# Performance work log

Hardware: AMD Instinct MI355X
Metric: run time of the kernel (lower is better)

## Reference

```python
import jax, jax.numpy as jnp
import numpy as np

D_MODEL = 1024
N_HEAD = 16
ATT_DIM = D_MODEL // N_HEAD  # 64
B, S = 8, 2048


def setup_inputs() -> dict:
    key = jax.random.key(0)
    kq, kk, kv, kwq, kwk, kwv = jax.random.split(key, 6)
    # xavier_uniform bound for Linear(hidden_dim -> att_dim)
    bound = float(np.sqrt(6.0 / (D_MODEL + ATT_DIM)))
    return {
        "q": jax.random.normal(kq, (B, S, D_MODEL), dtype=jnp.float32),
        "k": jax.random.normal(kk, (B, S, D_MODEL), dtype=jnp.float32),
        "v": jax.random.normal(kv, (B, S, D_MODEL), dtype=jnp.float32),
        "Wq": jax.random.uniform(kwq, (ATT_DIM, D_MODEL), jnp.float32, -bound, bound),
        "Wk": jax.random.uniform(kwk, (ATT_DIM, D_MODEL), jnp.float32, -bound, bound),
        "Wv": jax.random.uniform(kwv, (ATT_DIM, D_MODEL), jnp.float32, -bound, bound),
    }


def reference(q, k, v, Wq, Wk, Wv):
    # Linear projections (no bias): [B,S,d_model] @ [d_model,att_dim]
    qp = jnp.einsum('bsd,ed->bse', q, Wq)
    kp = jnp.einsum('bsd,ed->bse', k, Wk)
    vp = jnp.einsum('bsd,ed->bse', v, Wv)
    # Scores: note original divides by att_dim (not sqrt)
    scores = jnp.einsum('bqe,bke->bqk', qp, kp) / ATT_DIM
    probs = jax.nn.softmax(scores, axis=-1)  # [B,S,S]
    att = jnp.einsum('bqk,bke->bqe', probs, vp)  # [B,S,att_dim]
    # dropout is identity in eval mode
    return (att, probs)
```

## Files before the change

kernel.cpp:

```cpp
#include <hip/hip_runtime.h>
#include <hip/hip_bf16.h>

#define D_MODEL 1024
#define ATT_DIM 64
#define BATCH 8
#define SEQ 2048
#define MROWS (BATCH * SEQ)

typedef short bf16x8 __attribute__((ext_vector_type(8)));
typedef float f32x4 __attribute__((ext_vector_type(4)));

#define MFMA16(a, b, c) __builtin_amdgcn_mfma_f32_16x16x32_bf16((a), (b), (c), 0, 0, 0)

__device__ inline short f2bf(float f) {
    union { __hip_bfloat16 h; short s; } u;
    u.h = __float2bfloat16(f);
    return u.s;
}

__device__ __forceinline__ void gload_lds16(const float* g, float* l) {
    __builtin_amdgcn_global_load_lds(
        (const __attribute__((address_space(1))) void*)g,
        (__attribute__((address_space(3))) void*)l, 16, 0, 0);
}

__global__ __launch_bounds__(256) void wcvt_kernel(
    const float* __restrict__ Wq, const float* __restrict__ Wk,
    const float* __restrict__ Wv, short* __restrict__ Wbf)
{
    const int idx = blockIdx.x * 256 + threadIdx.x;
    const int per = ATT_DIM * D_MODEL;
    const int base = idx * 8;
    const int mi = base / per;
    const int off = base - mi * per;
    const float* src = (mi == 0) ? Wq : (mi == 1 ? Wk : Wv);
    const float sc = (mi == 0) ? (1.0f / 64.0f) : 1.0f;
    const float4 a = *reinterpret_cast<const float4*>(src + off);
    const float4 b = *reinterpret_cast<const float4*>(src + off + 4);
    bf16x8 r;
    r[0] = f2bf(a.x * sc); r[1] = f2bf(a.y * sc);
    r[2] = f2bf(a.z * sc); r[3] = f2bf(a.w * sc);
    r[4] = f2bf(b.x * sc); r[5] = f2bf(b.y * sc);
    r[6] = f2bf(b.z * sc); r[7] = f2bf(b.w * sc);
    *reinterpret_cast<bf16x8*>(Wbf + base) = r;
}

__global__ __launch_bounds__(256) void proj_mfma_kernel(
    const float* __restrict__ q, const float* __restrict__ k,
    const float* __restrict__ v, const short* __restrict__ Wbf,
    short* __restrict__ qp, short* __restrict__ kp, short* __restrict__ vpT)
{
    const int mat = blockIdx.y;
    const float* x = (mat == 0) ? q : (mat == 1 ? k : v);
    const short* W = Wbf + mat * ATT_DIM * D_MODEL;

    __shared__ float As[2][4096];

    const int tid = threadIdx.x;
    const int w = tid >> 6;
    const int l = tid & 63;
    const int lr = l & 15;
    const int g = l >> 4;

    const int m0 = blockIdx.x * 64;
    const int row = w * 16 + lr;
    const int xr = (row & 7) << 4;

    f32x4 acc[4] = {};

    #define STAGE(c, buf)                                                      \
        {                                                                      \
            const int kt_ = (c) * 64;                                          \
            _Pragma("unroll")                                                  \
            for (int j = 0; j < 4; ++j) {                                      \
                const int rs = (w * 4 + j) * 4 + g;                            \
                const int scb = (lr * 16) ^ ((rs & 7) << 4);                   \
                gload_lds16(x + (long)(m0 + rs) * D_MODEL + kt_ + (scb >> 2),  \
                            &As[buf][(w * 4 + j) * 256]);                      \
            }                                                                  \
        }

    STAGE(0, 0);
    __syncthreads();

    for (int c = 0; c < 16; ++c) {
        const int buf = c & 1;
        if (c < 15) STAGE(c + 1, buf ^ 1);

        const int kt = c * 64;
        const char* Ab = (const char*)&As[buf][0] + row * 256;
        #pragma unroll
        for (int ks = 0; ks < 2; ++ks) {
            const int b0 = ks * 128 + g * 32;
            const float4 a0 = *reinterpret_cast<const float4*>(Ab + (b0 ^ xr));
            const float4 a1 = *reinterpret_cast<const float4*>(Ab + ((b0 + 16) ^ xr));
            bf16x8 af;
            af[0] = f2bf(a0.x); af[1] = f2bf(a0.y); af[2] = f2bf(a0.z); af[3] = f2bf(a0.w);
            af[4] = f2bf(a1.x); af[5] = f2bf(a1.y); af[6] = f2bf(a1.z); af[7] = f2bf(a1.w);
            #pragma unroll
            for (int ef = 0; ef < 4; ++ef) {
                const bf16x8 wf = *reinterpret_cast<const bf16x8*>(
                    W + (ef * 16 + lr) * D_MODEL + kt + ks * 32 + g * 8);
                acc[ef] = MFMA16(af, wf, acc[ef]);
            }
        }
        __syncthreads();
    }
    #undef STAGE

    if (mat < 2) {
        short* out = (mat == 0) ? qp : kp;
        #pragma unroll
        for (int ef = 0; ef < 4; ++ef)
            #pragma unroll
            for (int j = 0; j < 4; ++j)
                out[(long)(m0 + w * 16 + g * 4 + j) * ATT_DIM + ef * 16 + lr] =
                    f2bf(acc[ef][j]);
    } else {
        const int b = m0 / SEQ;
        const int s0 = (m0 - b * SEQ) + w * 16;
        #pragma unroll
        for (int ef = 0; ef < 4; ++ef)
            #pragma unroll
            for (int j = 0; j < 4; ++j)
                vpT[((long)b * ATT_DIM + ef * 16 + lr) * SEQ + s0 + g * 4 + j] =
                    f2bf(acc[ef][j]);
    }
}

union AttnSmem {
    struct {
        short p[8][16][40];
        float m[8][16];
        float l[8][16];
    } a;
    float o[8][64][17];
};

__global__ __launch_bounds__(512) void attn_kernel(
    const short* __restrict__ qp, const short* __restrict__ kp,
    const short* __restrict__ vpT, float* __restrict__ probs,
    float* __restrict__ att)
{
    __shared__ AttnSmem lds;

    const int tid = threadIdx.x;
    const int w = tid >> 6;
    const int l = tid & 63;
    const int lr = l & 15;
    const int g = l >> 4;

    const int b = blockIdx.y;
    const int q0 = blockIdx.x * 16;

    const short* qpb = qp + ((long)b * SEQ + q0) * ATT_DIM;
    const short* kpb = kp + (long)b * SEQ * ATT_DIM;
    const short* vTb = vpT + (long)b * ATT_DIM * SEQ;

    const bf16x8 qa0 = *reinterpret_cast<const bf16x8*>(qpb + lr * ATT_DIM + g * 8);
    const bf16x8 qa1 = *reinterpret_cast<const bf16x8*>(qpb + lr * ATT_DIM + 32 + g * 8);

    const int kbeg = w * 256;

    f32x4 s[8][2];
    #pragma unroll
    for (int ch = 0; ch < 8; ++ch) {
        const short* kb = kpb + (long)(kbeg + ch * 32) * ATT_DIM;
        const bf16x8 kb00 = *reinterpret_cast<const bf16x8*>(kb + lr * ATT_DIM + g * 8);
        const bf16x8 kb01 = *reinterpret_cast<const bf16x8*>(kb + lr * ATT_DIM + 32 + g * 8);
        const bf16x8 kb10 = *reinterpret_cast<const bf16x8*>(kb + (16 + lr) * ATT_DIM + g * 8);
        const bf16x8 kb11 = *reinterpret_cast<const bf16x8*>(kb + (16 + lr) * ATT_DIM + 32 + g * 8);
        f32x4 t0 = {}; t0 = MFMA16(qa0, kb00, t0); t0 = MFMA16(qa1, kb01, t0);
        f32x4 t1 = {}; t1 = MFMA16(qa0, kb10, t1); t1 = MFMA16(qa1, kb11, t1);
        s[ch][0] = t0; s[ch][1] = t1;
    }

    float gm[4];
    #pragma unroll
    for (int j = 0; j < 4; ++j) {
        const float m0_ = fmaxf(fmaxf(s[0][0][j], s[0][1][j]), fmaxf(s[1][0][j], s[1][1][j]));
        const float m1_ = fmaxf(fmaxf(s[2][0][j], s[2][1][j]), fmaxf(s[3][0][j], s[3][1][j]));
        const float m2_ = fmaxf(fmaxf(s[4][0][j], s[4][1][j]), fmaxf(s[5][0][j], s[5][1][j]));
        const float m3_ = fmaxf(fmaxf(s[6][0][j], s[6][1][j]), fmaxf(s[7][0][j], s[7][1][j]));
        float mj = fmaxf(fmaxf(m0_, m1_), fmaxf(m2_, m3_));
        mj = fmaxf(mj, __shfl_xor(mj, 1));
        mj = fmaxf(mj, __shfl_xor(mj, 2));
        mj = fmaxf(mj, __shfl_xor(mj, 4));
        mj = fmaxf(mj, __shfl_xor(mj, 8));
        gm[j] = mj;
    }
    if (lr == 0) {
        #pragma unroll
        for (int j = 0; j < 4; ++j) lds.a.m[w][g * 4 + j] = gm[j];
    }
    __syncthreads();
    #pragma unroll
    for (int j = 0; j < 4; ++j) {
        const int qr = g * 4 + j;
        float mf = lds.a.m[0][qr];
        #pragma unroll
        for (int ww = 1; ww < 8; ++ww) mf = fmaxf(mf, lds.a.m[ww][qr]);
        gm[j] = mf;
    }

    float lsum[4] = {0.f, 0.f, 0.f, 0.f};
    #pragma unroll
    for (int ch = 0; ch < 8; ++ch)
        #pragma unroll
        for (int h = 0; h < 2; ++h)
            #pragma unroll
            for (int j = 0; j < 4; ++j) {
                const float e = __expf(s[ch][h][j] - gm[j]);
                s[ch][h][j] = e;
                lsum[j] += e;
            }
    #pragma unroll
    for (int j = 0; j < 4; ++j) {
        float lj = lsum[j];
        lj += __shfl_xor(lj, 1);
        lj += __shfl_xor(lj, 2);
        lj += __shfl_xor(lj, 4);
        lj += __shfl_xor(lj, 8);
        lsum[j] = lj;
    }
    if (lr == 0) {
        #pragma unroll
        for (int j = 0; j < 4; ++j) lds.a.l[w][g * 4 + j] = lsum[j];
    }
    __syncthreads();
    float invl[4];
    #pragma unroll
    for (int j = 0; j < 4; ++j) {
        const int qr = g * 4 + j;
        float lf = lds.a.l[0][qr];
        #pragma unroll
        for (int ww = 1; ww < 8; ++ww) lf += lds.a.l[ww][qr];
        invl[j] = 1.0f / lf;
    }

    f32x4 accO[4] = {};
    float* pbase = probs + ((long)b * SEQ + q0) * SEQ;

    #pragma unroll
    for (int ch = 0; ch < 8; ++ch) {
        const int k0 = kbeg + ch * 32;
        #pragma unroll
        for (int h = 0; h < 2; ++h)
            #pragma unroll
            for (int j = 0; j < 4; ++j) {
                const int qr = g * 4 + j;
                const float p = s[ch][h][j] * invl[j];
                pbase[(long)qr * SEQ + k0 + h * 16 + lr] = p;
                lds.a.p[w][qr][h * 16 + lr] = f2bf(p);
            }
        const bf16x8 pb = *reinterpret_cast<const bf16x8*>(&lds.a.p[w][lr][g * 8]);
        #pragma unroll
        for (int ef = 0; ef < 4; ++ef) {
            const bf16x8 va = *reinterpret_cast<const bf16x8*>(
                vTb + (long)(ef * 16 + lr) * SEQ + k0 + g * 8);
            accO[ef] = MFMA16(va, pb, accO[ef]);
        }
    }

    __syncthreads();
    #pragma unroll
    for (int ef = 0; ef < 4; ++ef)
        #pragma unroll
        for (int j = 0; j < 4; ++j)
            lds.o[w][ef * 16 + g * 4 + j][lr] = accO[ef][j];
    __syncthreads();

    {
        const int qr = tid >> 5;
        const int e0 = (tid & 31) * 2;
        float o0 = 0.f, o1 = 0.f;
        #pragma unroll
        for (int ww = 0; ww < 8; ++ww) {
            o0 += lds.o[ww][e0][qr];
            o1 += lds.o[ww][e0 + 1][qr];
        }
        float2 o = make_float2(o0, o1);
        *reinterpret_cast<float2*>(att + ((long)b * SEQ + q0 + qr) * ATT_DIM + e0) = o;
    }
}

extern "C" void kernel_launch(void* const* d_in, const int* in_sizes, int n_in,
                              void* d_out, int out_size, void* d_ws, size_t ws_size,
                              hipStream_t stream)
{
    const float* q  = (const float*)d_in[0];
    const float* k  = (const float*)d_in[1];
    const float* v  = (const float*)d_in[2];
    const float* Wq = (const float*)d_in[3];
    const float* Wk = (const float*)d_in[4];
    const float* Wv = (const float*)d_in[5];

    float* att   = (float*)d_out;
    float* probs = att + (size_t)BATCH * SEQ * ATT_DIM;

    short* qp  = (short*)d_ws;
    short* kp  = qp + (size_t)MROWS * ATT_DIM;
    short* vpT = kp + (size_t)MROWS * ATT_DIM;
    short* Wbf = vpT + (size_t)MROWS * ATT_DIM;

    wcvt_kernel<<<dim3(96), 256, 0, stream>>>(Wq, Wk, Wv, Wbf);

    proj_mfma_kernel<<<dim3(MROWS / 64, 3), 256, 0, stream>>>(
        q, k, v, Wbf, qp, kp, vpT);

    attn_kernel<<<dim3(SEQ / 16, BATCH), 512, 0, stream>>>(
        qp, kp, vpT, probs, att);
}
```

Measured before the change: 151.6 us.

## Use online softmax with QK recompute to cut register pressure

Replaces holding all 64 score values per lane in registers with an online max/sum pass over the key chunks, followed by a second pass that recomputes QK^T to produce the normalized probabilities. The final statistics are merged across waves with rescaled sums, which removes one block barrier. It also adds a min-blocks hint to launch_bounds so more waves can be resident. The cost is doubled QK MFMA work and K loads plus extra exps, and the unroll pragmas on the chunk loops are removed.

```diff
diff --git a/kernel.cpp b/kernel.cpp
--- a/kernel.cpp
+++ b/kernel.cpp
@@ -137,7 +137,7 @@
     float o[8][64][17];
 };
 
-__global__ __launch_bounds__(512) void attn_kernel(
+__global__ __launch_bounds__(512, 8) void attn_kernel(
     const short* __restrict__ qp, const short* __restrict__ kp,
     const short* __restrict__ vpT, float* __restrict__ probs,
     float* __restrict__ att)
@@ -162,8 +162,9 @@
 
     const int kbeg = w * 256;
 
-    f32x4 s[8][2];
-    #pragma unroll
+    float m[4] = {-1e30f, -1e30f, -1e30f, -1e30f};
+    float lsum[4] = {0.f, 0.f, 0.f, 0.f};
+
     for (int ch = 0; ch < 8; ++ch) {
         const short* kb = kpb + (long)(kbeg + ch * 32) * ATT_DIM;
         const bf16x8 kb00 = *reinterpret_cast<const bf16x8*>(kb + lr * ATT_DIM + g * 8);
@@ -172,87 +173,77 @@
         const bf16x8 kb11 = *reinterpret_cast<const bf16x8*>(kb + (16 + lr) * ATT_DIM + 32 + g * 8);
         f32x4 t0 = {}; t0 = MFMA16(qa0, kb00, t0); t0 = MFMA16(qa1, kb01, t0);
         f32x4 t1 = {}; t1 = MFMA16(qa0, kb10, t1); t1 = MFMA16(qa1, kb11, t1);
-        s[ch][0] = t0; s[ch][1] = t1;
-    }
-
-    float gm[4];
+        #pragma unroll
+        for (int j = 0; j < 4; ++j) {
+            const float cm = fmaxf(t0[j], t1[j]);
+            const float mn = fmaxf(m[j], cm);
+            lsum[j] = lsum[j] * __expf(m[j] - mn) +
+                      __expf(t0[j] - mn) + __expf(t1[j] - mn);
+            m[j] = mn;
+        }
+    }
+
     #pragma unroll
     for (int j = 0; j < 4; ++j) {
-        const float m0_ = fmaxf(fmaxf(s[0][0][j], s[0][1][j]), fmaxf(s[1][0][j], s[1][1][j]));
-        const float m1_ = fmaxf(fmaxf(s[2][0][j], s[2][1][j]), fmaxf(s[3][0][j], s[3][1][j]));
-        const float m2_ = fmaxf(fmaxf(s[4][0][j], s[4][1][j]), fmaxf(s[5][0][j], s[5][1][j]));
-        const float m3_ = fmaxf(fmaxf(s[6][0][j], s[6][1][j]), fmaxf(s[7][0][j], s[7][1][j]));
-        float mj = fmaxf(fmaxf(m0_, m1_), fmaxf(m2_, m3_));
+        float mj = m[j];
         mj = fmaxf(mj, __shfl_xor(mj, 1));
         mj = fmaxf(mj, __shfl_xor(mj, 2));
         mj = fmaxf(mj, __shfl_xor(mj, 4));
         mj = fmaxf(mj, __shfl_xor(mj, 8));
-        gm[j] = mj;
+        float lj = lsum[j] * __expf(m[j] - mj);
+        lj += __shfl_xor(lj, 1);
+        lj += __shfl_xor(lj, 2);
+        lj += __shfl_xor(lj, 4);
+        lj += __shfl_xor(lj, 8);
+        m[j] = mj; lsum[j] = lj;
     }
     if (lr == 0) {
         #pragma unroll
-        for (int j = 0; j < 4; ++j) lds.a.m[w][g * 4 + j] = gm[j];
+        for (int j = 0; j < 4; ++j) {
+            lds.a.m[w][g * 4 + j] = m[j];
+            lds.a.l[w][g * 4 + j] = lsum[j];
+        }
     }
     __syncthreads();
+
+    float gm[4], invl[4];
     #pragma unroll
     for (int j = 0; j < 4; ++j) {
         const int qr = g * 4 + j;
         float mf = lds.a.m[0][qr];
         #pragma unroll
         for (int ww = 1; ww < 8; ++ww) mf = fmaxf(mf, lds.a.m[ww][qr]);
+        float lf = 0.f;
+        #pragma unroll
+        for (int ww = 0; ww < 8; ++ww)
+            lf += lds.a.l[ww][qr] * __expf(lds.a.m[ww][qr] - mf);
         gm[j] = mf;
-    }
-
-    float lsum[4] = {0.f, 0.f, 0.f, 0.f};
-    #pragma unroll
-    for (int ch = 0; ch < 8; ++ch)
-        #pragma unroll
-        for (int h = 0; h < 2; ++h)
-            #pragma unroll
-            for (int j = 0; j < 4; ++j) {
-                const float e = __expf(s[ch][h][j] - gm[j]);
-                s[ch][h][j] = e;
-                lsum[j] += e;
-            }
-    #pragma unroll
-    for (int j = 0; j < 4; ++j) {
-        float lj = lsum[j];
-        lj += __shfl_xor(lj, 1);
-        lj += __shfl_xor(lj, 2);
-        lj += __shfl_xor(lj, 4);
-        lj += __shfl_xor(lj, 8);
-        lsum[j] = lj;
-    }
-    if (lr == 0) {
-        #pragma unroll
-        for (int j = 0; j < 4; ++j) lds.a.l[w][g * 4 + j] = lsum[j];
-    }
-    __syncthreads();
-    float invl[4];
-    #pragma unroll
-    for (int j = 0; j < 4; ++j) {
-        const int qr = g * 4 + j;
-        float lf = lds.a.l[0][qr];
-        #pragma unroll
-        for (int ww = 1; ww < 8; ++ww) lf += lds.a.l[ww][qr];
         invl[j] = 1.0f / lf;
     }
 
     f32x4 accO[4] = {};
     float* pbase = probs + ((long)b * SEQ + q0) * SEQ;
 
-    #pragma unroll
     for (int ch = 0; ch < 8; ++ch) {
         const int k0 = kbeg + ch * 32;
-        #pragma unroll
-        for (int h = 0; h < 2; ++h)
-            #pragma unroll
-            for (int j = 0; j < 4; ++j) {
-                const int qr = g * 4 + j;
-                const float p = s[ch][h][j] * invl[j];
-                pbase[(long)qr * SEQ + k0 + h * 16 + lr] = p;
-                lds.a.p[w][qr][h * 16 + lr] = f2bf(p);
-            }
+        const short* kb = kpb + (long)k0 * ATT_DIM;
+        const bf16x8 kb00 = *reinterpret_cast<const bf16x8*>(kb + lr * ATT_DIM + g * 8);
+        const bf16x8 kb01 = *reinterpret_cast<const bf16x8*>(kb + lr * ATT_DIM + 32 + g * 8);
+        const bf16x8 kb10 = *reinterpret_cast<const bf16x8*>(kb + (16 + lr) * ATT_DIM + g * 8);
+        const bf16x8 kb11 = *reinterpret_cast<const bf16x8*>(kb + (16 + lr) * ATT_DIM + 32 + g * 8);
+        f32x4 t0 = {}; t0 = MFMA16(qa0, kb00, t0); t0 = MFMA16(qa1, kb01, t0);
+        f32x4 t1 = {}; t1 = MFMA16(qa0, kb10, t1); t1 = MFMA16(qa1, kb11, t1);
+
+        #pragma unroll
+        for (int j = 0; j < 4; ++j) {
+            const int qr = g * 4 + j;
+            const float p0 = __expf(t0[j] - gm[j]) * invl[j];
+            const float p1 = __expf(t1[j] - gm[j]) * invl[j];
+            pbase[(long)qr * SEQ + k0 + lr] = p0;
+            pbase[(long)qr * SEQ + k0 + 16 + lr] = p1;
+            lds.a.p[w][qr][lr] = f2bf(p0);
+            lds.a.p[w][qr][16 + lr] = f2bf(p1);
+        }
         const bf16x8 pb = *reinterpret_cast<const bf16x8*>(&lds.a.p[w][lr][g * 8]);
         #pragma unroll
         for (int ef = 0; ef < 4; ++ef) {
```

Result: slower. 175.6 us (+15.8%).

## Transpose score MFMA layout, single-pass softmax stats, prefetch weight fragments

Applied to the files above, without the earlier changes.

The attention kernel swaps the MFMA operands so each lane holds four consecutive key scores for one query row. Probabilities can then be written as 16-byte vector stores instead of scalar stores. Softmax now computes the per-wave max and sum in one pass and merges them across waves with rescaling, which removes one block barrier and the second exp pass. Bf16 packing of P uses the packed convert instruction. The projection kernel also prefetches the next chunk's weight fragments into registers, at the cost of extra register pressure.

```diff
diff --git a/kernel.cpp b/kernel.cpp
--- a/kernel.cpp
+++ b/kernel.cpp
@@ -9,6 +9,7 @@
 
 typedef short bf16x8 __attribute__((ext_vector_type(8)));
 typedef float f32x4 __attribute__((ext_vector_type(4)));
+typedef long lx2 __attribute__((ext_vector_type(2)));
 
 #define MFMA16(a, b, c) __builtin_amdgcn_mfma_f32_16x16x32_bf16((a), (b), (c), 0, 0, 0)
 
@@ -16,6 +17,12 @@
     union { __hip_bfloat16 h; short s; } u;
     u.h = __float2bfloat16(f);
     return u.s;
+}
+
+__device__ __forceinline__ unsigned cvtpk(float lo, float hi) {
+    unsigned r;
+    asm("v_cvt_pk_bf16_f32 %0, %1, %2" : "=v"(r) : "v"(lo), "v"(hi));
+    return r;
 }
 
 __device__ __forceinline__ void gload_lds16(const float* g, float* l) {
@@ -80,14 +87,31 @@
             }                                                                  \
         }
 
+    #define WFRAG(c, ks, ef)                                                   \
+        (*reinterpret_cast<const bf16x8*>(                                     \
+            W + ((ef) * 16 + lr) * D_MODEL + (c) * 64 + (ks) * 32 + g * 8))
+
+    bf16x8 wreg[8];
+    #pragma unroll
+    for (int ks = 0; ks < 2; ++ks)
+        #pragma unroll
+        for (int ef = 0; ef < 4; ++ef) wreg[ks * 4 + ef] = WFRAG(0, ks, ef);
+
     STAGE(0, 0);
     __syncthreads();
 
     for (int c = 0; c < 16; ++c) {
         const int buf = c & 1;
-        if (c < 15) STAGE(c + 1, buf ^ 1);
-
-        const int kt = c * 64;
+        bf16x8 wnext[8];
+        if (c < 15) {
+            STAGE(c + 1, buf ^ 1);
+            #pragma unroll
+            for (int ks = 0; ks < 2; ++ks)
+                #pragma unroll
+                for (int ef = 0; ef < 4; ++ef)
+                    wnext[ks * 4 + ef] = WFRAG(c + 1, ks, ef);
+        }
+
         const char* Ab = (const char*)&As[buf][0] + row * 256;
         #pragma unroll
         for (int ks = 0; ks < 2; ++ks) {
@@ -98,15 +122,17 @@
             af[0] = f2bf(a0.x); af[1] = f2bf(a0.y); af[2] = f2bf(a0.z); af[3] = f2bf(a0.w);
             af[4] = f2bf(a1.x); af[5] = f2bf(a1.y); af[6] = f2bf(a1.z); af[7] = f2bf(a1.w);
             #pragma unroll
-            for (int ef = 0; ef < 4; ++ef) {
-                const bf16x8 wf = *reinterpret_cast<const bf16x8*>(
-                    W + (ef * 16 + lr) * D_MODEL + kt + ks * 32 + g * 8);
-                acc[ef] = MFMA16(af, wf, acc[ef]);
-            }
+            for (int ef = 0; ef < 4; ++ef)
+                acc[ef] = MFMA16(af, wreg[ks * 4 + ef], acc[ef]);
         }
         __syncthreads();
+        if (c < 15) {
+            #pragma unroll
+            for (int i = 0; i < 8; ++i) wreg[i] = wnext[i];
+        }
     }
     #undef STAGE
+    #undef WFRAG
 
     if (mat < 2) {
         short* out = (mat == 0) ? qp : kp;
@@ -129,11 +155,7 @@
 }
 
 union AttnSmem {
-    struct {
-        short p[8][16][40];
-        float m[8][16];
-        float l[8][16];
-    } a;
+    short pk[8][16][40];
     float o[8][64][17];
 };
 
@@ -142,7 +164,9 @@
     const short* __restrict__ vpT, float* __restrict__ probs,
     float* __restrict__ att)
 {
-    __shared__ AttnSmem lds;
+    __shared__ __align__(16) AttnSmem u;
+    __shared__ float stats_m[8][16];
+    __shared__ float stats_l[8][16];
 
     const int tid = threadIdx.x;
     const int w = tid >> 6;
@@ -170,90 +194,76 @@
         const bf16x8 kb01 = *reinterpret_cast<const bf16x8*>(kb + lr * ATT_DIM + 32 + g * 8);
         const bf16x8 kb10 = *reinterpret_cast<const bf16x8*>(kb + (16 + lr) * ATT_DIM + g * 8);
         const bf16x8 kb11 = *reinterpret_cast<const bf16x8*>(kb + (16 + lr) * ATT_DIM + 32 + g * 8);
-        f32x4 t0 = {}; t0 = MFMA16(qa0, kb00, t0); t0 = MFMA16(qa1, kb01, t0);
-        f32x4 t1 = {}; t1 = MFMA16(qa0, kb10, t1); t1 = MFMA16(qa1, kb11, t1);
+        f32x4 t0 = {}; t0 = MFMA16(kb00, qa0, t0); t0 = MFMA16(kb01, qa1, t0);
+        f32x4 t1 = {}; t1 = MFMA16(kb10, qa0, t1); t1 = MFMA16(kb11, qa1, t1);
         s[ch][0] = t0; s[ch][1] = t1;
     }
 
-    float gm[4];
-    #pragma unroll
-    for (int j = 0; j < 4; ++j) {
-        const float m0_ = fmaxf(fmaxf(s[0][0][j], s[0][1][j]), fmaxf(s[1][0][j], s[1][1][j]));
-        const float m1_ = fmaxf(fmaxf(s[2][0][j], s[2][1][j]), fmaxf(s[3][0][j], s[3][1][j]));
-        const float m2_ = fmaxf(fmaxf(s[4][0][j], s[4][1][j]), fmaxf(s[5][0][j], s[5][1][j]));
-        const float m3_ = fmaxf(fmaxf(s[6][0][j], s[6][1][j]), fmaxf(s[7][0][j], s[7][1][j]));
-        float mj = fmaxf(fmaxf(m0_, m1_), fmaxf(m2_, m3_));
-        mj = fmaxf(mj, __shfl_xor(mj, 1));
-        mj = fmaxf(mj, __shfl_xor(mj, 2));
-        mj = fmaxf(mj, __shfl_xor(mj, 4));
-        mj = fmaxf(mj, __shfl_xor(mj, 8));
-        gm[j] = mj;
-    }
-    if (lr == 0) {
-        #pragma unroll
-        for (int j = 0; j < 4; ++j) lds.a.m[w][g * 4 + j] = gm[j];
-    }
+    float mw = -1e30f;
+    #pragma unroll
+    for (int ch = 0; ch < 8; ++ch)
+        #pragma unroll
+        for (int h = 0; h < 2; ++h)
+            mw = fmaxf(mw, fmaxf(fmaxf(s[ch][h][0], s[ch][h][1]),
+                                 fmaxf(s[ch][h][2], s[ch][h][3])));
+    mw = fmaxf(mw, __shfl_xor(mw, 16));
+    mw = fmaxf(mw, __shfl_xor(mw, 32));
+
+    float lw = 0.f;
+    #pragma unroll
+    for (int ch = 0; ch < 8; ++ch)
+        #pragma unroll
+        for (int h = 0; h < 2; ++h)
+            #pragma unroll
+            for (int j = 0; j < 4; ++j) {
+                const float e = __expf(s[ch][h][j] - mw);
+                s[ch][h][j] = e;
+                lw += e;
+            }
+    lw += __shfl_xor(lw, 16);
+    lw += __shfl_xor(lw, 32);
+
+    if (l < 16) { stats_m[w][l] = mw; stats_l[w][l] = lw; }
     __syncthreads();
-    #pragma unroll
-    for (int j = 0; j < 4; ++j) {
-        const int qr = g * 4 + j;
-        float mf = lds.a.m[0][qr];
-        #pragma unroll
-        for (int ww = 1; ww < 8; ++ww) mf = fmaxf(mf, lds.a.m[ww][qr]);
-        gm[j] = mf;
-    }
-
-    float lsum[4] = {0.f, 0.f, 0.f, 0.f};
+
+    float gm = stats_m[0][lr];
+    #pragma unroll
+    for (int ww = 1; ww < 8; ++ww) gm = fmaxf(gm, stats_m[ww][lr]);
+    float tot = 0.f;
+    #pragma unroll
+    for (int ww = 0; ww < 8; ++ww)
+        tot += stats_l[ww][lr] * __expf(stats_m[ww][lr] - gm);
+    const float scale = __expf(mw - gm) / tot;
     #pragma unroll
     for (int ch = 0; ch < 8; ++ch)
         #pragma unroll
         for (int h = 0; h < 2; ++h)
-            #pragma unroll
-            for (int j = 0; j < 4; ++j) {
-                const float e = __expf(s[ch][h][j] - gm[j]);
-                s[ch][h][j] = e;
-                lsum[j] += e;
-            }
-    #pragma unroll
-    for (int j = 0; j < 4; ++j) {
-        float lj = lsum[j];
-        lj += __shfl_xor(lj, 1);
-        lj += __shfl_xor(lj, 2);
-        lj += __shfl_xor(lj, 4);
-        lj += __shfl_xor(lj, 8);
-        lsum[j] = lj;
-    }
-    if (lr == 0) {
-        #pragma unroll
-        for (int j = 0; j < 4; ++j) lds.a.l[w][g * 4 + j] = lsum[j];
-    }
-    __syncthreads();
-    float invl[4];
-    #pragma unroll
-    for (int j = 0; j < 4; ++j) {
-        const int qr = g * 4 + j;
-        float lf = lds.a.l[0][qr];
-        #pragma unroll
-        for (int ww = 1; ww < 8; ++ww) lf += lds.a.l[ww][qr];
-        invl[j] = 1.0f / lf;
-    }
+            s[ch][h] *= scale;
 
     f32x4 accO[4] = {};
-    float* pbase = probs + ((long)b * SEQ + q0) * SEQ;
+    float* pbase = probs + ((long)b * SEQ + q0 + lr) * SEQ;
 
     #pragma unroll
     for (int ch = 0; ch < 8; ++ch) {
         const int k0 = kbeg + ch * 32;
-        #pragma unroll
-        for (int h = 0; h < 2; ++h)
-            #pragma unroll
-            for (int j = 0; j < 4; ++j) {
-                const int qr = g * 4 + j;
-                const float p = s[ch][h][j] * invl[j];
-                pbase[(long)qr * SEQ + k0 + h * 16 + lr] = p;
-                lds.a.p[w][qr][h * 16 + lr] = f2bf(p);
-            }
-        const bf16x8 pb = *reinterpret_cast<const bf16x8*>(&lds.a.p[w][lr][g * 8]);
+        *reinterpret_cast<f32x4*>(pbase + k0 + g * 4)      = s[ch][0];
+        *reinterpret_cast<f32x4*>(pbase + k0 + 16 + g * 4) = s[ch][1];
+
+        uint4 cc;
+        cc.x = cvtpk(s[ch][0][0], s[ch][0][1]);
+        cc.y = cvtpk(s[ch][0][2], s[ch][0][3]);
+        cc.z = cvtpk(s[ch][1][0], s[ch][1][1]);
+        cc.w = cvtpk(s[ch][1][2], s[ch][1][3]);
+        *reinterpret_cast<uint4*>(&u.pk[w][lr][g * 8]) = cc;
+
+        const long lo = *reinterpret_cast<const long*>(
+            &u.pk[w][lr][(2 * (g & 1)) * 8 + (g >> 1) * 4]);
+        const long hi = *reinterpret_cast<const long*>(
+            &u.pk[w][lr][(2 * (g & 1) + 1) * 8 + (g >> 1) * 4]);
+        union { lx2 l2; bf16x8 v; } pbu;
+        pbu.l2[0] = lo; pbu.l2[1] = hi;
+        const bf16x8 pb = pbu.v;
+
         #pragma unroll
         for (int ef = 0; ef < 4; ++ef) {
             const bf16x8 va = *reinterpret_cast<const bf16x8*>(
@@ -267,7 +277,7 @@
     for (int ef = 0; ef < 4; ++ef)
         #pragma unroll
         for (int j = 0; j < 4; ++j)
-            lds.o[w][ef * 16 + g * 4 + j][lr] = accO[ef][j];
+            u.o[w][ef * 16 + g * 4 + j][lr] = accO[ef][j];
     __syncthreads();
 
     {
@@ -276,8 +286,8 @@
         float o0 = 0.f, o1 = 0.f;
         #pragma unroll
         for (int ww = 0; ww < 8; ++ww) {
-            o0 += lds.o[ww][e0][qr];
-            o1 += lds.o[ww][e0 + 1][qr];
+            o0 += u.o[ww][e0][qr];
+            o1 += u.o[ww][e0 + 1][qr];
         }
         float2 o = make_float2(o0, o1);
         *reinterpret_cast<float2*>(att + ((long)b * SEQ + q0 + qr) * ATT_DIM + e0) = o;
```

Result: no change. 151.2 us (-0.3%).
